# Optimization experiments

Hardware: AMD Instinct MI355X
Metric: run time of the kernel (lower is better)

Reference implementation:

```python
import jax, jax.numpy as jnp
import numpy as np


def _lstm_layer(x_seq, h0, c0, Wih, Whh, bih, bhh):
    """Standard (PyTorch-gate-order: i, f, g, o) LSTM over a [T, B, C] sequence."""
    b = bih + bhh  # [4H]
    # Precompute input projections for all timesteps at once: [T, B, 4H]
    x_proj = jnp.einsum('tbc,gc->tbg', x_seq, Wih) + b

    def step(carry, xp_t):
        h, c = carry
        gates = xp_t + h @ Whh.T  # [B, 4H]
        i, f, g, o = jnp.split(gates, 4, axis=-1)
        i = jax.nn.sigmoid(i)
        f = jax.nn.sigmoid(f)
        g = jnp.tanh(g)
        o = jax.nn.sigmoid(o)
        c_new = f * c + i * g
        h_new = o * jnp.tanh(c_new)
        return (h_new, c_new), h_new

    (hT, cT), ys = jax.lax.scan(step, (h0, c0), x_proj)
    return ys, hT, cT


def setup_inputs() -> dict:
    key = jax.random.key(0)
    ks = jax.random.split(key, 16)
    T, B, C, H = 1024, 64, 256, 512
    s_in = 1.0 / np.sqrt(H)
    inp = {
        'x': jax.random.normal(ks[0], (T, B, C), jnp.float32),
        'h0_0': jax.random.normal(ks[1], (B, H), jnp.float32) * 0.1,
        'c0_0': jax.random.normal(ks[2], (B, H), jnp.float32) * 0.1,
        'h0_1': jax.random.normal(ks[3], (B, H), jnp.float32) * 0.1,
        'c0_1': jax.random.normal(ks[4], (B, H), jnp.float32) * 0.1,
        'Wih0': jax.random.normal(ks[5], (4 * H, C), jnp.float32) * s_in,
        'Whh0': jax.random.normal(ks[6], (4 * H, H), jnp.float32) * s_in,
        'bih0': jax.random.normal(ks[7], (4 * H,), jnp.float32) * s_in,
        'bhh0': jax.random.normal(ks[8], (4 * H,), jnp.float32) * s_in,
        'Wih1': jax.random.normal(ks[9], (4 * H, H), jnp.float32) * s_in,
        'Whh1': jax.random.normal(ks[10], (4 * H, H), jnp.float32) * s_in,
        'bih1': jax.random.normal(ks[11], (4 * H,), jnp.float32) * s_in,
        'bhh1': jax.random.normal(ks[12], (4 * H,), jnp.float32) * s_in,
    }
    return inp


def reference(x, h0_0, c0_0, h0_1, c0_1, Wih0, Whh0, bih0, bhh0, Wih1, Whh1, bih1, bhh1):
    # Layer 0 over the full sequence, then layer 1 consumes its outputs.
    # Mathematically identical to the original timestep-major Python loop.
    y0, h1f, c1f = _lstm_layer(x, h0_0, c0_0, Wih0, Whh0, bih0, bhh0)
    y1, h2f, c2f = _lstm_layer(y0, h0_1, c0_1, Wih1, Whh1, bih1, bhh1)
    return (y1, h1f, c1f, h2f, c2f)
```

## Files before the change

### kernel.cpp

```cpp
#include <hip/hip_runtime.h>


#define TT 1024
#define BB 64
#define CC 256
#define HH 512
#define Y_ELEMS (TT * BB * HH)
#define S_ELEMS (BB * HH)

typedef __attribute__((ext_vector_type(8))) short bf16x8;
typedef __attribute__((ext_vector_type(4))) float f32x4;
typedef unsigned int u32;
typedef unsigned short u16;
typedef unsigned long long u64;

#define WS_BAR 0
#define WS_GEN 32768
#define WS_BSUM0 36864
#define WS_BSUM1 45056
#define WS_H0 53248
#define WS_H1 184320
#define WS_WPK0 315392
#define WS_WPK1 3461120

__device__ __forceinline__ u16 f2b_rne(float f) {
    u32 u = __float_as_uint(f);
    return (u16)((u + 0x7FFFu + ((u >> 16) & 1u)) >> 16);
}
__device__ __forceinline__ u16 f2b_fast(float f) {
    return (u16)((__float_as_uint(f) + 0x8000u) >> 16);
}
__device__ __forceinline__ float sigf(float z) { return 1.0f / (1.0f + __expf(-z)); }
__device__ __forceinline__ float tanh_f(float z) { return 2.0f / (1.0f + __expf(-2.0f * z)) - 1.0f; }

__device__ __forceinline__ bf16x8 pack8(float4 a, float4 b) {
    union { u16 u[8]; bf16x8 v; } r;
    r.u[0] = f2b_fast(a.x); r.u[1] = f2b_fast(a.y); r.u[2] = f2b_fast(a.z); r.u[3] = f2b_fast(a.w);
    r.u[4] = f2b_fast(b.x); r.u[5] = f2b_fast(b.y); r.u[6] = f2b_fast(b.z); r.u[7] = f2b_fast(b.w);
    return r.v;
}

__device__ __forceinline__ u32 ld_u32_sc(const u32* p) {
    return __hip_atomic_load(p, __ATOMIC_RELAXED, __HIP_MEMORY_SCOPE_AGENT);
}
__device__ __forceinline__ void st_u32_sc(u32* p, u32 v) {
    __hip_atomic_store(p, v, __ATOMIC_RELAXED, __HIP_MEMORY_SCOPE_AGENT);
}

__global__ void k_init(const float* __restrict__ bih0, const float* __restrict__ bhh0,
                       const float* __restrict__ bih1, const float* __restrict__ bhh1,
                       const float* __restrict__ h00, const float* __restrict__ h01,
                       unsigned char* __restrict__ ws) {
    u32* bar = (u32*)(ws + WS_BAR);
    float* bs0 = (float*)(ws + WS_BSUM0);
    float* bs1 = (float*)(ws + WS_BSUM1);
    u16* h0 = (u16*)(ws + WS_H0);
    u16* h1 = (u16*)(ws + WS_H1);
    int t = blockIdx.x * 256 + threadIdx.x;
    if (t < 8448) bar[t] = 0u;
    if (t < 2048) { bs0[t] = bih0[t] + bhh0[t]; bs1[t] = bih1[t] + bhh1[t]; }
    if (t < S_ELEMS) {
        int b = t >> 9, col = t & 511;
        int no = ((col >> 2) << 8) + (b << 2) + (col & 3);
        h0[no] = f2b_rne(h00[t]);
        h1[no] = f2b_rne(h01[t]);
    }
}

__global__ void k_wprep(const float* __restrict__ Wih0, const float* __restrict__ Whh0,
                        const float* __restrict__ Wih1, const float* __restrict__ Whh1,
                        unsigned char* __restrict__ ws) {
    u16* wpk0 = (u16*)(ws + WS_WPK0);
    u16* wpk1 = (u16*)(ws + WS_WPK1);
    int u = blockIdx.x * 256 + threadIdx.x;
    const float* s;
    u16* d;
    if (u < 128 * 24 * 64) {
        int bidL = u / (24 * 64);
        int kt = (u >> 6) % 24;
        int lane = u & 63;
        int n = lane & 15, quad = lane >> 4;
        int row = (n >> 2) * 512 + bidL * 4 + (n & 3);
        int k = kt * 32 + quad * 8;
        s = (k < 256) ? (Wih0 + (size_t)row * 256 + k) : (Whh0 + (size_t)row * 512 + (k - 256));
        d = wpk0 + (size_t)((bidL * 24 + kt) * 64 + lane) * 8;
    } else {
        int v = u - 128 * 24 * 64;
        int bidL = v / (32 * 64);
        int kt = (v >> 6) % 32;
        int lane = v & 63;
        int n = lane & 15, quad = lane >> 4;
        int row = (n >> 2) * 512 + bidL * 4 + (n & 3);
        int k = kt * 32 + quad * 8;
        s = (k < 512) ? (Wih1 + (size_t)row * 512 + k) : (Whh1 + (size_t)row * 512 + (k - 512));
        d = wpk1 + (size_t)((bidL * 32 + kt) * 64 + lane) * 8;
    }
    #pragma unroll
    for (int i = 0; i < 8; ++i) d[i] = f2b_rne(s[i]);
}

template <int LAYER>
__device__ void run_ticks(const float* __restrict__ x, const float* __restrict__ c0,
                          float* __restrict__ out, unsigned char* __restrict__ ws, int bidL) {
    constexpr int NKT = (LAYER == 0) ? 24 : 32;
    u32* slots = (u32*)(ws + WS_BAR);
    u32* gen = (u32*)(ws + WS_GEN);
    const float* bs = (const float*)(ws + (LAYER == 0 ? WS_BSUM0 : WS_BSUM1));
    u16* h0base = (u16*)(ws + WS_H0);
    u16* h1base = (u16*)(ws + WS_H1);
    const u16* wpk = (const u16*)(ws + (LAYER == 0 ? WS_WPK0 : WS_WPK1));

    const int tid = threadIdx.x, lane = tid & 63, wave = tid >> 6;
    const int r16 = lane & 15, quad = lane >> 4, q8 = quad * 8;
    const int gg = r16 >> 2, jj = r16 & 3;
    const int b0 = wave * 16;
    const int col = bidL * 4 + jj;
    const int myb = b0 + quad * 4 + gg;
    const int sl0 = (quad << 4) | (0 << 2) | jj;
    const int sl1 = (quad << 4) | (1 << 2) | jj;
    const int sl2 = (quad << 4) | (2 << 2) | jj;
    const int sl3 = (quad << 4) | (3 << 2) | jj;
    const int baseln = (quad << 4) | (gg << 2);

    const size_t cbase = (size_t)quad * 1024 + (size_t)(b0 + r16) * 8;

    const float bi = bs[0 * HH + col], bf_ = bs[1 * HH + col];
    const float bg = bs[2 * HH + col], bo = bs[3 * HH + col];
    float c = c0[myb * HH + col];

    f32x4 wf[NKT];
    {
        const u16* wp = wpk + (size_t)(bidL * NKT * 64 + lane) * 8;
        #pragma unroll
        for (int kt = 0; kt < NKT; ++kt) wf[kt] = *(const f32x4*)(wp + (size_t)kt * 64 * 8);
        #pragma unroll
        for (int kt = 0; kt < NKT; ++kt) asm volatile("" : "+v"(wf[kt]));
    }

    float4 xf0[8], xf1[8];
    if (LAYER == 0) {
        const float* xp = x + (size_t)(b0 + r16) * CC + q8;
        #pragma unroll
        for (int kt = 0; kt < 8; ++kt) {
            xf0[kt] = *(const float4*)(xp + kt * 32);
            xf1[kt] = *(const float4*)(xp + kt * 32 + 4);
        }
    }

    for (int i = 0; i <= TT; ++i) {
        const bool active = (LAYER == 0) ? (i < TT) : (i >= 1);
        const int t = (LAYER == 0) ? i : i - 1;
        float h = 0.f;
        if (active) {
            f32x4 a0 = {0.f,0.f,0.f,0.f}, a1 = {0.f,0.f,0.f,0.f};
            f32x4 a2 = {0.f,0.f,0.f,0.f}, a3 = {0.f,0.f,0.f,0.f};
            if (LAYER == 0) {
                u64 alo[16], ahi[16];
                {
                    const char* hb = (const char*)(h0base + (size_t)(t & 1) * S_ELEMS) + cbase;
                    #pragma unroll
                    for (int kt = 0; kt < 16; ++kt) {
                        const char* pk = hb + kt * 4096;
                        asm volatile("global_load_dwordx2 %0, %1, off sc0 sc1"
                                     : "=&v"(alo[kt]) : "v"(pk) : "memory");
                        asm volatile("global_load_dwordx2 %0, %1, off offset:512 sc0 sc1"
                                     : "=&v"(ahi[kt]) : "v"(pk) : "memory");
                    }
                }
                #pragma unroll
                for (int kt = 0; kt < 8; ++kt) {
                    bf16x8 a = pack8(xf0[kt], xf1[kt]);
                    bf16x8 wv = __builtin_bit_cast(bf16x8, wf[kt]);
                    f32x4& dst = (kt & 2) ? ((kt & 1) ? a3 : a2) : ((kt & 1) ? a1 : a0);
                    dst = __builtin_amdgcn_mfma_f32_16x16x32_bf16(a, wv, dst, 0, 0, 0);
                }
                asm volatile("s_waitcnt vmcnt(0)" ::: "memory");
                __builtin_amdgcn_sched_barrier(0);
                #pragma unroll
                for (int kt = 0; kt < 16; ++kt) {
                    union { u64 q[2]; bf16x8 v; } fa;
                    fa.q[0] = alo[kt]; fa.q[1] = ahi[kt];
                    bf16x8 wv = __builtin_bit_cast(bf16x8, wf[8 + kt]);
                    f32x4& dst = (kt & 2) ? ((kt & 1) ? a3 : a2) : ((kt & 1) ? a1 : a0);
                    dst = __builtin_amdgcn_mfma_f32_16x16x32_bf16(fa.v, wv, dst, 0, 0, 0);
                }
            } else {
                u64 plo[16], phi[16], qlo[16], qhi[16];
                {
                    const char* ha = (const char*)(h0base + (size_t)((t + 1) & 1) * S_ELEMS) + cbase;
                    const char* hb = (const char*)(h1base + (size_t)(t & 1) * S_ELEMS) + cbase;
                    #pragma unroll
                    for (int kt = 0; kt < 16; ++kt) {
                        const char* pk = hb + kt * 4096;
                        asm volatile("global_load_dwordx2 %0, %1, off sc0 sc1"
                                     : "=&v"(qlo[kt]) : "v"(pk) : "memory");
                        asm volatile("global_load_dwordx2 %0, %1, off offset:512 sc0 sc1"
                                     : "=&v"(qhi[kt]) : "v"(pk) : "memory");
                    }
                    #pragma unroll
                    for (int kt = 0; kt < 16; ++kt) {
                        const char* pk = ha + kt * 4096;
                        asm volatile("global_load_dwordx2 %0, %1, off sc0 sc1"
                                     : "=&v"(plo[kt]) : "v"(pk) : "memory");
                        asm volatile("global_load_dwordx2 %0, %1, off offset:512 sc0 sc1"
                                     : "=&v"(phi[kt]) : "v"(pk) : "memory");
                    }
                }
                asm volatile("s_waitcnt vmcnt(0)" ::: "memory");
                __builtin_amdgcn_sched_barrier(0);
                #pragma unroll
                for (int kt = 0; kt < 32; ++kt) {
                    union { u64 q[2]; bf16x8 v; } fa;
                    if (kt < 16) { fa.q[0] = plo[kt]; fa.q[1] = phi[kt]; }
                    else         { fa.q[0] = qlo[kt - 16]; fa.q[1] = qhi[kt - 16]; }
                    bf16x8 wv = __builtin_bit_cast(bf16x8, wf[kt]);
                    f32x4& dst = (kt & 2) ? ((kt & 1) ? a3 : a2) : ((kt & 1) ? a1 : a0);
                    dst = __builtin_amdgcn_mfma_f32_16x16x32_bf16(fa.v, wv, dst, 0, 0, 0);
                }
            }
            f32x4 acc = (a0 + a1) + (a2 + a3);

            float gi = 0.f, gf = 0.f, gc = 0.f, go = 0.f;
            #pragma unroll
            for (int r = 0; r < 4; ++r) {
                float v0 = __shfl(acc[r], sl0, 64);
                float v1 = __shfl(acc[r], sl1, 64);
                float v2 = __shfl(acc[r], sl2, 64);
                float v3 = __shfl(acc[r], sl3, 64);
                if (r == gg) { gi = v0; gf = v1; gc = v2; go = v3; }
            }
            gi = sigf(gi + bi);
            gf = sigf(gf + bf_);
            gc = tanh_f(gc + bg);
            go = sigf(go + bo);
            c = gf * c + gi * gc;
            h = go * tanh_f(c);

            u32 w0 = f2b_rne(h);
            u32 w1 = (u32)__shfl((int)w0, baseln + 1, 64);
            u32 w2 = (u32)__shfl((int)w0, baseln + 2, 64);
            u32 w3 = (u32)__shfl((int)w0, baseln + 3, 64);
            if (jj == 0) {
                u64 pkd = (u64)(w0 | (w1 << 16)) | ((u64)(w2 | (w3 << 16)) << 32);
                u64* hw = (u64*)((LAYER == 0 ? h0base : h1base)
                                 + (size_t)((t + 1) & 1) * S_ELEMS)
                          + (size_t)bidL * 64 + myb;
                __hip_atomic_store(hw, pkd, __ATOMIC_RELAXED, __HIP_MEMORY_SCOPE_AGENT);
            }
        }
        if (i < TT) {
            asm volatile("s_waitcnt vmcnt(0)" ::: "memory");
            __syncthreads();
            if (tid == 0)
                st_u32_sc(&slots[(u32)blockIdx.x * 32], (u32)(i + 1));
        }
        if (active) {
            if (LAYER == 1) out[(size_t)t * S_ELEMS + myb * HH + col] = h;
            if (t == TT - 1) {
                float* fin = out + Y_ELEMS + (LAYER == 0 ? 0 : 2) * S_ELEMS;
                fin[myb * HH + col] = h;
                fin[S_ELEMS + myb * HH + col] = c;
            }
        }
        if (LAYER == 0 && i + 1 < TT) {
            const float* xp = x + ((size_t)(i + 1) * BB + b0 + r16) * CC + q8;
            #pragma unroll
            for (int kt = 0; kt < 8; ++kt) {
                xf0[kt] = *(const float4*)(xp + kt * 32);
                xf1[kt] = *(const float4*)(xp + kt * 32 + 4);
            }
        }
        if (i < TT) {
            const u32 tgt = (u32)(i + 1);
            if (blockIdx.x == 0) {
                if (tid < 64) {
                    const u32* p0 = slots + ((u32)tid * 4 + 0) * 32;
                    const u32* p1 = slots + ((u32)tid * 4 + 1) * 32;
                    const u32* p2 = slots + ((u32)tid * 4 + 2) * 32;
                    const u32* p3 = slots + ((u32)tid * 4 + 3) * 32;
                    u32 m;
                    do {
                        u32 va = ld_u32_sc(p0);
                        u32 vb = ld_u32_sc(p1);
                        u32 vc = ld_u32_sc(p2);
                        u32 vd = ld_u32_sc(p3);
                        m = min(min(va, vb), min(vc, vd));
                    } while (m < tgt);
                }
                __syncthreads();
                if (tid == 0) {
                    #pragma unroll
                    for (int k2 = 0; k2 < 4; ++k2) st_u32_sc(gen + k2 * 32, tgt);
                }
            } else {
                if (tid == 0) {
                    const u32* gp = gen + ((u32)blockIdx.x & 3) * 32;
                    while (ld_u32_sc(gp) < tgt) { }
                }
                __syncthreads();
            }
        }
    }
}

__global__ __launch_bounds__(256) __attribute__((amdgpu_waves_per_eu(1, 1)))
void k_lstm(const float* __restrict__ x,
            const float* __restrict__ c00,
            const float* __restrict__ c01,
            float* __restrict__ out,
            unsigned char* __restrict__ ws) {
    const int bid = blockIdx.x;
    if (bid < 128) run_ticks<0>(x, c00, out, ws, bid);
    else           run_ticks<1>(x, c01, out, ws, bid - 128);
}

extern "C" void kernel_launch(void* const* d_in, const int* in_sizes, int n_in,
                              void* d_out, int out_size, void* d_ws, size_t ws_size,
                              hipStream_t stream) {
    const float* x    = (const float*)d_in[0];
    const float* h0_0 = (const float*)d_in[1];
    const float* c0_0 = (const float*)d_in[2];
    const float* h0_1 = (const float*)d_in[3];
    const float* c0_1 = (const float*)d_in[4];
    const float* Wih0 = (const float*)d_in[5];
    const float* Whh0 = (const float*)d_in[6];
    const float* bih0 = (const float*)d_in[7];
    const float* bhh0 = (const float*)d_in[8];
    const float* Wih1 = (const float*)d_in[9];
    const float* Whh1 = (const float*)d_in[10];
    const float* bih1 = (const float*)d_in[11];
    const float* bhh1 = (const float*)d_in[12];
    float* out = (float*)d_out;
    unsigned char* ws = (unsigned char*)d_ws;

    k_init<<<128, 256, 0, stream>>>(bih0, bhh0, bih1, bhh1, h0_0, h0_1, ws);
    k_wprep<<<1792, 256, 0, stream>>>(Wih0, Whh0, Wih1, Whh1, ws);
    k_lstm<<<256, 256, 0, stream>>>(x, c0_0, c0_1, out, ws);
}
```

Measured before the change: 5.149 ms.

## Stage packed LSTM weights in LDS and vectorize layer-1 output stores

Each block now copies its packed bf16 weight slice into shared memory once at startup, and every timestep reads MFMA B-operands from LDS instead of holding 24–32 f32x4 values in VGPRs. This lowers register pressure, which may let the compiler schedule the many in-flight h loads better. The cost is an LDS read per MFMA on the serial critical path of every step. Separately, layer-1 output writes gather four adjacent columns with shuffles and issue one float4 store instead of four scalar stores.

```diff
diff --git a/kernel.cpp b/kernel.cpp
--- a/kernel.cpp
+++ b/kernel.cpp
@@ -101,7 +101,8 @@
 
 template <int LAYER>
 __device__ void run_ticks(const float* __restrict__ x, const float* __restrict__ c0,
-                          float* __restrict__ out, unsigned char* __restrict__ ws, int bidL) {
+                          float* __restrict__ out, unsigned char* __restrict__ ws,
+                          int bidL, u16* wlds) {
     constexpr int NKT = (LAYER == 0) ? 24 : 32;
     u32* slots = (u32*)(ws + WS_BAR);
     u32* gen = (u32*)(ws + WS_GEN);
@@ -124,18 +125,17 @@
 
     const size_t cbase = (size_t)quad * 1024 + (size_t)(b0 + r16) * 8;
 
+    {
+        const u16* src = wpk + (size_t)(bidL * NKT * 64) * 8;
+        for (int ofs = tid * 8; ofs < NKT * 512; ofs += 256 * 8)
+            *(f32x4*)(wlds + ofs) = *(const f32x4*)(src + ofs);
+        __syncthreads();
+    }
+    const u16* wl = wlds + (size_t)lane * 8;
+
     const float bi = bs[0 * HH + col], bf_ = bs[1 * HH + col];
     const float bg = bs[2 * HH + col], bo = bs[3 * HH + col];
     float c = c0[myb * HH + col];
-
-    f32x4 wf[NKT];
-    {
-        const u16* wp = wpk + (size_t)(bidL * NKT * 64 + lane) * 8;
-        #pragma unroll
-        for (int kt = 0; kt < NKT; ++kt) wf[kt] = *(const f32x4*)(wp + (size_t)kt * 64 * 8);
-        #pragma unroll
-        for (int kt = 0; kt < NKT; ++kt) asm volatile("" : "+v"(wf[kt]));
-    }
 
     float4 xf0[8], xf1[8];
     if (LAYER == 0) {
@@ -170,7 +170,7 @@
                 #pragma unroll
                 for (int kt = 0; kt < 8; ++kt) {
                     bf16x8 a = pack8(xf0[kt], xf1[kt]);
-                    bf16x8 wv = __builtin_bit_cast(bf16x8, wf[kt]);
+                    bf16x8 wv = *(const bf16x8*)(wl + (size_t)kt * 512);
                     f32x4& dst = (kt & 2) ? ((kt & 1) ? a3 : a2) : ((kt & 1) ? a1 : a0);
                     dst = __builtin_amdgcn_mfma_f32_16x16x32_bf16(a, wv, dst, 0, 0, 0);
                 }
@@ -180,7 +180,7 @@
                 for (int kt = 0; kt < 16; ++kt) {
                     union { u64 q[2]; bf16x8 v; } fa;
                     fa.q[0] = alo[kt]; fa.q[1] = ahi[kt];
-                    bf16x8 wv = __builtin_bit_cast(bf16x8, wf[8 + kt]);
+                    bf16x8 wv = *(const bf16x8*)(wl + (size_t)(8 + kt) * 512);
                     f32x4& dst = (kt & 2) ? ((kt & 1) ? a3 : a2) : ((kt & 1) ? a1 : a0);
                     dst = __builtin_amdgcn_mfma_f32_16x16x32_bf16(fa.v, wv, dst, 0, 0, 0);
                 }
@@ -213,7 +213,7 @@
                     union { u64 q[2]; bf16x8 v; } fa;
                     if (kt < 16) { fa.q[0] = plo[kt]; fa.q[1] = phi[kt]; }
                     else         { fa.q[0] = qlo[kt - 16]; fa.q[1] = qhi[kt - 16]; }
-                    bf16x8 wv = __builtin_bit_cast(bf16x8, wf[kt]);
+                    bf16x8 wv = *(const bf16x8*)(wl + (size_t)kt * 512);
                     f32x4& dst = (kt & 2) ? ((kt & 1) ? a3 : a2) : ((kt & 1) ? a1 : a0);
                     dst = __builtin_amdgcn_mfma_f32_16x16x32_bf16(fa.v, wv, dst, 0, 0, 0);
                 }
@@ -255,7 +255,15 @@
                 st_u32_sc(&slots[(u32)blockIdx.x * 32], (u32)(i + 1));
         }
         if (active) {
-            if (LAYER == 1) out[(size_t)t * S_ELEMS + myb * HH + col] = h;
+            if (LAYER == 1) {
+                float o1 = __shfl(h, baseln + 1, 64);
+                float o2 = __shfl(h, baseln + 2, 64);
+                float o3 = __shfl(h, baseln + 3, 64);
+                if (jj == 0) {
+                    float4 ov = { h, o1, o2, o3 };
+                    *(float4*)(out + (size_t)t * S_ELEMS + (size_t)myb * HH + bidL * 4) = ov;
+                }
+            }
             if (t == TT - 1) {
                 float* fin = out + Y_ELEMS + (LAYER == 0 ? 0 : 2) * S_ELEMS;
                 fin[myb * HH + col] = h;
@@ -309,9 +317,10 @@
             const float* __restrict__ c01,
             float* __restrict__ out,
             unsigned char* __restrict__ ws) {
+    __shared__ __align__(16) u16 wlds[16384];
     const int bid = blockIdx.x;
-    if (bid < 128) run_ticks<0>(x, c00, out, ws, bid);
-    else           run_ticks<1>(x, c01, out, ws, bid - 128);
+    if (bid < 128) run_ticks<0>(x, c00, out, ws, bid, wlds);
+    else           run_ticks<1>(x, c01, out, ws, bid - 128, wlds);
 }
 
 extern "C" void kernel_launch(void* const* d_in, const int* in_sizes, int n_in,
```

New measurement: 5.524 ms. +7.3%, slower.

## Replace centralized grid barrier with sharded atomic counters and split MFMA wait

Applied to the files above, without the earlier changes.

Replaces the two-level barrier (block 0 polls per-block slots, then broadcasts a generation flag) with 8 sharded atomic counters. Each block increments one shard and polls all eight directly, which removes a serial hop from every timestep's grid sync. The MFMAs on the first-issued half of the h loads now start as soon as those loads land, overlapping with the rest of the loads. Layer-1 output stores are gathered across lanes via shuffles into float4 writes. The new barrier adds atomic contention on the shared counters and more polling traffic from all 256 blocks.

```diff
diff --git a/kernel.cpp b/kernel.cpp
--- a/kernel.cpp
+++ b/kernel.cpp
@@ -15,7 +15,7 @@
 typedef unsigned long long u64;
 
 #define WS_BAR 0
-#define WS_GEN 32768
+#define WS_CNT 32768
 #define WS_BSUM0 36864
 #define WS_BSUM1 45056
 #define WS_H0 53248
@@ -43,8 +43,8 @@
 __device__ __forceinline__ u32 ld_u32_sc(const u32* p) {
     return __hip_atomic_load(p, __ATOMIC_RELAXED, __HIP_MEMORY_SCOPE_AGENT);
 }
-__device__ __forceinline__ void st_u32_sc(u32* p, u32 v) {
-    __hip_atomic_store(p, v, __ATOMIC_RELAXED, __HIP_MEMORY_SCOPE_AGENT);
+__device__ __forceinline__ void add_u32_sc(u32* p, u32 v) {
+    (void)__hip_atomic_fetch_add(p, v, __ATOMIC_RELAXED, __HIP_MEMORY_SCOPE_AGENT);
 }
 
 __global__ void k_init(const float* __restrict__ bih0, const float* __restrict__ bhh0,
@@ -103,8 +103,7 @@
 __device__ void run_ticks(const float* __restrict__ x, const float* __restrict__ c0,
                           float* __restrict__ out, unsigned char* __restrict__ ws, int bidL) {
     constexpr int NKT = (LAYER == 0) ? 24 : 32;
-    u32* slots = (u32*)(ws + WS_BAR);
-    u32* gen = (u32*)(ws + WS_GEN);
+    u32* cnt = (u32*)(ws + WS_CNT);
     const float* bs = (const float*)(ws + (LAYER == 0 ? WS_BSUM0 : WS_BSUM1));
     u16* h0base = (u16*)(ws + WS_H0);
     u16* h1base = (u16*)(ws + WS_H1);
@@ -123,6 +122,8 @@
     const int baseln = (quad << 4) | (gg << 2);
 
     const size_t cbase = (size_t)quad * 1024 + (size_t)(b0 + r16) * 8;
+
+    u32* mycnt = cnt + ((u32)blockIdx.x & 7) * 32;
 
     const float bi = bs[0 * HH + col], bf_ = bs[1 * HH + col];
     const float bg = bs[2 * HH + col], bo = bs[3 * HH + col];
@@ -206,13 +207,22 @@
                                      : "=&v"(phi[kt]) : "v"(pk) : "memory");
                     }
                 }
+                asm volatile("s_waitcnt vmcnt(32)" ::: "memory");
+                __builtin_amdgcn_sched_barrier(0);
+                #pragma unroll
+                for (int kt = 16; kt < 32; ++kt) {
+                    union { u64 q[2]; bf16x8 v; } fa;
+                    fa.q[0] = qlo[kt - 16]; fa.q[1] = qhi[kt - 16];
+                    bf16x8 wv = __builtin_bit_cast(bf16x8, wf[kt]);
+                    f32x4& dst = (kt & 2) ? ((kt & 1) ? a3 : a2) : ((kt & 1) ? a1 : a0);
+                    dst = __builtin_amdgcn_mfma_f32_16x16x32_bf16(fa.v, wv, dst, 0, 0, 0);
+                }
                 asm volatile("s_waitcnt vmcnt(0)" ::: "memory");
                 __builtin_amdgcn_sched_barrier(0);
                 #pragma unroll
-                for (int kt = 0; kt < 32; ++kt) {
+                for (int kt = 0; kt < 16; ++kt) {
                     union { u64 q[2]; bf16x8 v; } fa;
-                    if (kt < 16) { fa.q[0] = plo[kt]; fa.q[1] = phi[kt]; }
-                    else         { fa.q[0] = qlo[kt - 16]; fa.q[1] = qhi[kt - 16]; }
+                    fa.q[0] = plo[kt]; fa.q[1] = phi[kt];
                     bf16x8 wv = __builtin_bit_cast(bf16x8, wf[kt]);
                     f32x4& dst = (kt & 2) ? ((kt & 1) ? a3 : a2) : ((kt & 1) ? a1 : a0);
                     dst = __builtin_amdgcn_mfma_f32_16x16x32_bf16(fa.v, wv, dst, 0, 0, 0);
@@ -251,11 +261,18 @@
         if (i < TT) {
             asm volatile("s_waitcnt vmcnt(0)" ::: "memory");
             __syncthreads();
-            if (tid == 0)
-                st_u32_sc(&slots[(u32)blockIdx.x * 32], (u32)(i + 1));
+            if (tid == 0) add_u32_sc(mycnt, 1u);
         }
         if (active) {
-            if (LAYER == 1) out[(size_t)t * S_ELEMS + myb * HH + col] = h;
+            if (LAYER == 1) {
+                float o1 = __shfl(h, baseln + 1, 64);
+                float o2 = __shfl(h, baseln + 2, 64);
+                float o3 = __shfl(h, baseln + 3, 64);
+                if (jj == 0) {
+                    float4 ov = { h, o1, o2, o3 };
+                    *(float4*)(out + (size_t)t * S_ELEMS + (size_t)myb * HH + bidL * 4) = ov;
+                }
+            }
             if (t == TT - 1) {
                 float* fin = out + Y_ELEMS + (LAYER == 0 ? 0 : 2) * S_ELEMS;
                 fin[myb * HH + col] = h;
@@ -271,34 +288,23 @@
             }
         }
         if (i < TT) {
-            const u32 tgt = (u32)(i + 1);
-            if (blockIdx.x == 0) {
-                if (tid < 64) {
-                    const u32* p0 = slots + ((u32)tid * 4 + 0) * 32;
-                    const u32* p1 = slots + ((u32)tid * 4 + 1) * 32;
-                    const u32* p2 = slots + ((u32)tid * 4 + 2) * 32;
-                    const u32* p3 = slots + ((u32)tid * 4 + 3) * 32;
-                    u32 m;
-                    do {
-                        u32 va = ld_u32_sc(p0);
-                        u32 vb = ld_u32_sc(p1);
-                        u32 vc = ld_u32_sc(p2);
-                        u32 vd = ld_u32_sc(p3);
-                        m = min(min(va, vb), min(vc, vd));
-                    } while (m < tgt);
-                }
-                __syncthreads();
-                if (tid == 0) {
-                    #pragma unroll
-                    for (int k2 = 0; k2 < 4; ++k2) st_u32_sc(gen + k2 * 32, tgt);
-                }
-            } else {
-                if (tid == 0) {
-                    const u32* gp = gen + ((u32)blockIdx.x & 3) * 32;
-                    while (ld_u32_sc(gp) < tgt) { }
-                }
-                __syncthreads();
-            }
+            const u32 tgt = (u32)(i + 1) * 32u;
+            if (tid == 0) {
+                while (true) {
+                    u32 v0 = ld_u32_sc(cnt + 0 * 32);
+                    u32 v1 = ld_u32_sc(cnt + 1 * 32);
+                    u32 v2 = ld_u32_sc(cnt + 2 * 32);
+                    u32 v3 = ld_u32_sc(cnt + 3 * 32);
+                    u32 v4 = ld_u32_sc(cnt + 4 * 32);
+                    u32 v5 = ld_u32_sc(cnt + 5 * 32);
+                    u32 v6 = ld_u32_sc(cnt + 6 * 32);
+                    u32 v7 = ld_u32_sc(cnt + 7 * 32);
+                    u32 m = min(min(min(v0, v1), min(v2, v3)),
+                                min(min(v4, v5), min(v6, v7)));
+                    if (m >= tgt) break;
+                }
+            }
+            __syncthreads();
         }
     }
 }
```

Result: faster. 4.984 ms (-3.2%).
